# Kernel optimization log

Measured on AMD Instinct MI355X. Metric: run time of the kernel, lower is better.

The kernel has to match this reference:

```python
import jax, jax.numpy as jnp
import numpy as np

B, N, F = 2, 512, 64
LN_EPS = 1e-6

def _ln(x, scale, bias):
    mu = jnp.mean(x, axis=-1, keepdims=True)
    var = jnp.mean(jnp.square(x - mu), axis=-1, keepdims=True)
    return (x - mu) * jax.lax.rsqrt(var + LN_EPS) * scale + bias

def setup_inputs() -> dict:
    key = jax.random.key(0)
    k = jax.random.split(key, 16)
    w = lambda kk, s: jax.random.normal(kk, s, jnp.float32) * 0.02
    return {
        'qs': jax.random.normal(k[0], (B, N, F), jnp.float32),
        'ks': jax.random.normal(k[1], (B, N, F), jnp.float32),
        'vs': jax.random.normal(k[2], (B, N, F), jnp.float32),
        'qs_s': jax.random.normal(k[3], (B, N, 2), jnp.float32),
        'ks_s': jax.random.normal(k[4], (B, N, 2), jnp.float32),
        'qs_t': jax.random.uniform(k[5], (B, N, 1), dtype=jnp.float32),
        'ks_t': jax.random.uniform(k[6], (B, N, 1), dtype=jnp.float32),
        'valid_lens': jax.random.randint(k[7], (B,), 1, N + 1),
        'Wv': w(k[8], (F, 64)), 'bv': jnp.zeros((64,), jnp.float32),
        'Wa1': w(k[9], (2 * F + 5, 256)), 'ba1': jnp.zeros((256,), jnp.float32),
        'Wa2': w(k[10], (256, 256)), 'ba2': jnp.zeros((256,), jnp.float32),
        'Wa3': w(k[11], (256, 1)), 'ba3': jnp.zeros((1,), jnp.float32),
        'Wg1': w(k[12], (64, 256)), 'bg1': jnp.zeros((256,), jnp.float32),
        'Wg2': w(k[13], (256, 64)), 'bg2': jnp.zeros((64,), jnp.float32),
        'ln1_s': jnp.ones((64,), jnp.float32), 'ln1_b': jnp.zeros((64,), jnp.float32),
        'ln2_s': jnp.ones((64,), jnp.float32), 'ln2_b': jnp.zeros((64,), jnp.float32),
    }

def reference(qs, ks, vs, qs_s, ks_s, qs_t, ks_t, valid_lens,
              Wv, bv, Wa1, ba1, Wa2, ba2, Wa3, ba3,
              Wg1, bg1, Wg2, bg2, ln1_s, ln1_b, ln2_s, ln2_b):
    Bb, Q, Ff = qs.shape
    K = ks.shape[1]
    # pairwise broadcast-concat features: (B, Q, K, 2F+5)
    qb = jnp.broadcast_to(qs[:, :, None, :], (Bb, Q, K, Ff))
    kb = jnp.broadcast_to(ks[:, None, :, :], (Bb, Q, K, Ff))
    s_diff = qs_s[:, :, None, :] - ks_s[:, None, :, :]            # (B,Q,K,2)
    s_dist = jnp.linalg.norm(s_diff, axis=-1, keepdims=True)      # (B,Q,K,1)
    t_diff = qs_t[:, :, None, :] - ks_t[:, None, :, :]            # (B,Q,K,1)
    m = jnp.concatenate([qb, kb, s_diff, s_dist, jnp.square(s_dist), t_diff], axis=-1)
    # validity mask over the node axis (Q == K node-set attention)
    v_mask = (jnp.arange(K)[None, :] < valid_lens[:, None])[..., None]  # (B,K,1)
    mask = jnp.logical_and(v_mask, t_diff[..., 0] > 0)                   # (B,Q,K)
    # per-pair MLP attention score
    h = jax.nn.gelu(m @ Wa1 + ba1)
    h = jax.nn.gelu(h @ Wa2 + ba2)
    attn = (h @ Wa3 + ba3)[..., 0]                                       # (B,Q,K)
    attn = jnp.where(mask, attn, 0.0)
    vproj = vs @ Wv + bv                                                 # (B,K,64)
    ctx = _ln(jnp.einsum('bqk,bkd->bqd', attn, vproj), ln1_s, ln1_b)     # (B,Q,64)
    gate = jax.nn.gelu(ctx @ Wg1 + bg1) @ Wg2 + bg2                      # (B,Q,64)
    pooled = jnp.max(jnp.where(v_mask, gate * ctx, -jnp.inf), axis=1)    # (B,64)
    vnode = _ln(pooled, ln2_s, ln2_b)
    return ctx, vnode
```

## Files before the change

kernel.cpp:

```cpp
#include <hip/hip_runtime.h>
#include <math.h>

#define BB 2
#define NN 512
#define FF 64
#define HH 256
#define LN_EPS 1e-6f

typedef __attribute__((ext_vector_type(8))) short short8v;
typedef __attribute__((ext_vector_type(4))) float float4v;

#define LDAH 264

__device__ __forceinline__ float gelu_tanh(float x) {
    float x2 = x * x;
    float t  = __builtin_fmaf(0.10294340f, x2, 2.30211830f);
    float e  = exp2f(x * t);
    float r  = __builtin_amdgcn_rcpf(e + 1.0f);
    return __builtin_fmaf(-x, r, x);
}

__device__ __forceinline__ unsigned short f2bf(float f) {
    unsigned u = __float_as_uint(f);
    unsigned r = u + 0x7fffu + ((u >> 16) & 1u);
    return (unsigned short)(r >> 16);
}

__global__ __launch_bounds__(256) void prep_kernel(
    const float* __restrict__ qs, const float* __restrict__ ks,
    const float* __restrict__ vs,
    const float* __restrict__ Wa1, const float* __restrict__ ba1,
    const float* __restrict__ Wv,  const float* __restrict__ bv,
    const float* __restrict__ Wa2,
    const float* __restrict__ qs_t, const float* __restrict__ ks_t,
    const int*   __restrict__ valid_lens,
    float* __restrict__ Aq, float* __restrict__ Ak,
    float* __restrict__ vproj, unsigned short* __restrict__ Wa2T,
    int* __restrict__ klist, int* __restrict__ wl_count, int* __restrict__ wl,
    float* __restrict__ ctx_zero) {
    __shared__ int s_cnt[8];
    __shared__ int s_off[9];
    const int bid = blockIdx.x;
    const int t   = threadIdx.x;
    if (bid < 1024) {
        int idx = bid * 256 + t;
        int j  = idx & (HH - 1);
        int bn = idx >> 8;
        const float* qrow = qs + bn * FF;
        const float* krow = ks + bn * FF;
        float aq = ba1[j];
        float ak = 0.0f;
#pragma unroll 8
        for (int f = 0; f < FF; ++f) {
            aq += qrow[f] * Wa1[f * HH + j];
            ak += krow[f] * Wa1[(FF + f) * HH + j];
        }
        Aq[idx] = aq;
        Ak[idx] = ak;
    } else if (bid < 1280) {
        int idx = (bid - 1024) * 256 + t;
        int d  = idx & 63;
        int bn = idx >> 6;
        const float* vrow = vs + bn * FF;
        float a = bv[d];
#pragma unroll 8
        for (int f = 0; f < FF; ++f) a += vrow[f] * Wv[f * 64 + d];
        vproj[idx] = a;
        ctx_zero[idx] = 0.0f;
    } else if (bid < 1536) {
        int idx = (bid - 1280) * 256 + t;
        int n = idx >> 8;
        int i = idx & 255;
        Wa2T[idx] = f2bf(Wa2[i * HH + n]);
    } else {
        const int bq = bid - 1536;
        const int b  = bq >> 9;
        const int q  = bq & 511;
        if (q >= valid_lens[b]) return;
        const float qt = qs_t[bq];
        const int lane = t & 63;
        const int w    = t >> 6;
        bool validr[2];
        int  posr[2];
#pragma unroll
        for (int r = 0; r < 2; ++r) {
            int k = r * 256 + t;
            float kt = ks_t[b * NN + k];
            bool valid = (qt - kt) > 0.0f;
            unsigned long long bal = __ballot(valid);
            validr[r] = valid;
            posr[r] = (int)__popcll(bal & ((1ull << lane) - 1ull));
            if (lane == 0) s_cnt[r * 4 + w] = (int)__popcll(bal);
        }
        __syncthreads();
        if (t == 0) {
            int acc = 0;
#pragma unroll
            for (int i = 0; i < 8; ++i) { s_off[i] = acc; acc += s_cnt[i]; }
            s_off[8] = acc;
        }
        __syncthreads();
#pragma unroll
        for (int r = 0; r < 2; ++r)
            if (validr[r])
                klist[bq * 512 + s_off[r * 4 + w] + posr[r]] = r * 256 + t;
        const int nk = s_off[8];
        if (t == 0 && nk > 0) {
            int nch = (nk + 63) >> 6;
            int base = atomicAdd(wl_count, nch);
            for (int c = 0; c < nch; ++c) {
                int nv = nk - (c << 6);
                nv = nv > 64 ? 64 : nv;
                wl[base + c] = bq | (c << 10) | (nv << 13);
            }
        }
    }
}

__global__ __launch_bounds__(256, 3) void attn_ctx_kernel(
    const float* __restrict__ ks_s, const float* __restrict__ qs_s,
    const float* __restrict__ qs_t, const float* __restrict__ ks_t,
    const float* __restrict__ Wa1,
    const unsigned short* __restrict__ Wa2T,
    const float* __restrict__ ba2, const float* __restrict__ Wa3,
    const float* __restrict__ ba3,
    const float* __restrict__ Aq,  const float* __restrict__ Ak,
    const float* __restrict__ vproj,
    const int* __restrict__ klist, const int* __restrict__ wl_count,
    const int* __restrict__ wl,
    float* __restrict__ ctx_acc_g) {

    __shared__ unsigned short s_h1[64 * LDAH];
    __shared__ float4 s_feat4[64];
    __shared__ int    s_koe[64];
    __shared__ int    s_kvo[64];
    __shared__ float  s_part[4 * 64];
    __shared__ float  s_attn[64];

    const int i = blockIdx.x;
    if (i >= wl_count[0]) return;

    const int t    = threadIdx.x;
    const int lane = t & 63;
    const int w    = t >> 6;
    const int l15  = lane & 15;
    const int quad = lane >> 4;

    const int e  = wl[i];
    const int bq = e & 1023;
    const int c  = (e >> 10) & 7;
    const int nv = (e >> 13) & 127;
    const int b  = bq >> 9;

    const int n0 = w * 64;
    const unsigned short* bbase = Wa2T + (size_t)(n0 + l15) * HH + quad * 8;
    short8v Bcur[4];
#pragma unroll
    for (int nt = 0; nt < 4; ++nt)
        Bcur[nt] = *(const short8v*)(bbase + (size_t)nt * 16 * HH);

    const float qt   = qs_t[bq];
    const float qss0 = qs_s[bq * 2 + 0];
    const float qss1 = qs_s[bq * 2 + 1];
    if (t < 64) {
        int k = klist[bq * 512 + c * 64 + ((t < nv) ? t : 0)];
        int bk = b * NN + k;
        float d0 = qss0 - ks_s[bk * 2 + 0];
        float d1 = qss1 - ks_s[bk * 2 + 1];
        float dist = sqrtf(d0 * d0 + d1 * d1);
        float td = qt - ks_t[bk];
        s_feat4[t] = make_float4(d0, d1, dist, td);
        s_koe[t] = bk * HH;
        s_kvo[t] = bk * 64;
    }
    __syncthreads();

    {
        const int j = t;
        const float aq_j = Aq[bq * HH + j];
        const float wx0 = Wa1[128 * HH + j];
        const float wx1 = Wa1[129 * HH + j];
        const float wx2 = Wa1[130 * HH + j];
        const float wx3 = Wa1[131 * HH + j];
        const float wx4 = Wa1[132 * HH + j];
        const float* __restrict__ Akj = Ak + j;
#pragma unroll
        for (int g = 0; g < 8; ++g) {
            float akv[8];
#pragma unroll
            for (int u = 0; u < 8; ++u)
                akv[u] = Akj[s_koe[g * 8 + u]];
#pragma unroll
            for (int u = 0; u < 8; ++u) {
                int kl = g * 8 + u;
                float4 f = s_feat4[kl];
                float v = aq_j + akv[u] + wx0 * f.x + wx1 * f.y + wx2 * f.z
                        + wx3 * (f.z * f.z) + wx4 * f.w;
                s_h1[kl * LDAH + j] = f2bf(gelu_tanh(v));
            }
        }
    }
    __syncthreads();

    float4v acc[4][4];
#pragma unroll
    for (int mt = 0; mt < 4; ++mt)
#pragma unroll
        for (int nt = 0; nt < 4; ++nt) acc[mt][nt] = (float4v){0.f, 0.f, 0.f, 0.f};
    const unsigned short* abase = s_h1 + l15 * LDAH + quad * 8;
#pragma unroll
    for (int ksx = 0; ksx < 8; ++ksx) {
        short8v Bnxt[4];
        if (ksx < 7) {
            const int k1 = (ksx + 1) * 32;
#pragma unroll
            for (int nt = 0; nt < 4; ++nt)
                Bnxt[nt] = *(const short8v*)(bbase + (size_t)nt * 16 * HH + k1);
        }
        short8v Af[4];
        const int k0 = ksx * 32;
#pragma unroll
        for (int mt = 0; mt < 4; ++mt)
            Af[mt] = *(const short8v*)(abase + mt * 16 * LDAH + k0);
#pragma unroll
        for (int mt = 0; mt < 4; ++mt)
#pragma unroll
            for (int nt = 0; nt < 4; ++nt)
                acc[mt][nt] = __builtin_amdgcn_mfma_f32_16x16x32_bf16(
                    Af[mt], Bcur[nt], acc[mt][nt], 0, 0, 0);
        if (ksx < 7) {
#pragma unroll
            for (int nt = 0; nt < 4; ++nt) Bcur[nt] = Bnxt[nt];
        }
    }

    {
        float ba2r[4], wa3r[4];
#pragma unroll
        for (int nt = 0; nt < 4; ++nt) {
            int col = n0 + nt * 16 + l15;
            ba2r[nt] = ba2[col];
            wa3r[nt] = Wa3[col];
        }
        float prow[4][4];
#pragma unroll
        for (int mt = 0; mt < 4; ++mt)
#pragma unroll
            for (int r = 0; r < 4; ++r) prow[mt][r] = 0.0f;
#pragma unroll
        for (int mt = 0; mt < 4; ++mt)
#pragma unroll
            for (int nt = 0; nt < 4; ++nt)
#pragma unroll
                for (int r = 0; r < 4; ++r)
                    prow[mt][r] += gelu_tanh(acc[mt][nt][r] + ba2r[nt]) * wa3r[nt];
#pragma unroll
        for (int m = 1; m < 16; m <<= 1)
#pragma unroll
            for (int mt = 0; mt < 4; ++mt)
#pragma unroll
                for (int r = 0; r < 4; ++r)
                    prow[mt][r] += __shfl_xor(prow[mt][r], m);
        if (l15 == 0) {
#pragma unroll
            for (int mt = 0; mt < 4; ++mt)
#pragma unroll
                for (int r = 0; r < 4; ++r)
                    s_part[w * 64 + mt * 16 + quad * 4 + r] = prow[mt][r];
        }
    }
    __syncthreads();

    if (t < 64) {
        float a = 0.0f;
        if (t < nv)
            a = s_part[t] + s_part[64 + t] + s_part[128 + t] + s_part[192 + t] + ba3[0];
        s_attn[t] = a;
    }
    __syncthreads();

    {
        float cacc = 0.0f;
#pragma unroll
        for (int g = 0; g < 2; ++g) {
            float vv[8];
#pragma unroll
            for (int u = 0; u < 8; ++u)
                vv[u] = vproj[s_kvo[w * 16 + g * 8 + u] + lane];
#pragma unroll
            for (int u = 0; u < 8; ++u)
                cacc += s_attn[w * 16 + g * 8 + u] * vv[u];
        }
        s_part[w * 64 + lane] = cacc;
    }
    __syncthreads();
    if (t < 64) {
        float v = s_part[t] + s_part[64 + t] + s_part[128 + t] + s_part[192 + t];
        atomicAdd(&ctx_acc_g[bq * 64 + t], v);
    }
}

__global__ __launch_bounds__(256) void gate_kernel(
    float* __restrict__ ctx,
    const float* __restrict__ ln1_s, const float* __restrict__ ln1_b,
    const float* __restrict__ Wg1, const float* __restrict__ bg1,
    const float* __restrict__ Wg2, const float* __restrict__ bg2,
    const int* __restrict__ valid_lens,
    float* __restrict__ gctx) {
    __shared__ float s_ctx[64];
    __shared__ float s_hg[256];
    const int t  = threadIdx.x;
    const int bq = blockIdx.x;
    const int b  = bq >> 9;
    const int q  = bq & 511;
    if (t < 64) {
        float x = ctx[bq * 64 + t];
        float s = x;
#pragma unroll
        for (int m = 1; m < 64; m <<= 1) s += __shfl_xor(s, m);
        float mu = s * (1.0f / 64.0f);
        float dv = x - mu;
        float vv = dv * dv;
#pragma unroll
        for (int m = 1; m < 64; m <<= 1) vv += __shfl_xor(vv, m);
        float rs = rsqrtf(vv * (1.0f / 64.0f) + LN_EPS);
        float y = dv * rs * ln1_s[t] + ln1_b[t];
        ctx[bq * 64 + t] = y;
        s_ctx[t] = y;
    }
    __syncthreads();
    float a = bg1[t];
#pragma unroll 8
    for (int d = 0; d < 64; ++d) a += s_ctx[d] * Wg1[d * 256 + t];
    s_hg[t] = gelu_tanh(a);
    __syncthreads();
    if (t < 64) {
        float g = bg2[t];
#pragma unroll 8
        for (int jj = 0; jj < 256; ++jj) g += s_hg[jj] * Wg2[jj * 64 + t];
        float val = g * s_ctx[t];
        if (q >= valid_lens[b]) val = -INFINITY;
        gctx[bq * 64 + t] = val;
    }
}

__global__ __launch_bounds__(256) void pool_kernel(
    const float* __restrict__ gctx,
    const float* __restrict__ ln2_s, const float* __restrict__ ln2_b,
    float* __restrict__ vnode_out) {
    __shared__ float s_red[4 * 64];
    const int t = threadIdx.x;
    const int b = blockIdx.x;
    const int d = t & 63;
    const int g = t >> 6;
    float m = -INFINITY;
#pragma unroll 4
    for (int q = g; q < NN; q += 4)
        m = fmaxf(m, gctx[(b * NN + q) * 64 + d]);
    s_red[g * 64 + d] = m;
    __syncthreads();
    if (t < 64) {
        float x = fmaxf(fmaxf(s_red[t], s_red[64 + t]),
                        fmaxf(s_red[128 + t], s_red[192 + t]));
        float s = x;
#pragma unroll
        for (int mm = 1; mm < 64; mm <<= 1) s += __shfl_xor(s, mm);
        float mu = s * (1.0f / 64.0f);
        float dv = x - mu;
        float vv = dv * dv;
#pragma unroll
        for (int mm = 1; mm < 64; mm <<= 1) vv += __shfl_xor(vv, mm);
        float rs = rsqrtf(vv * (1.0f / 64.0f) + LN_EPS);
        vnode_out[b * 64 + t] = dv * rs * ln2_s[t] + ln2_b[t];
    }
}

extern "C" void kernel_launch(void* const* d_in, const int* in_sizes, int n_in,
                              void* d_out, int out_size, void* d_ws, size_t ws_size,
                              hipStream_t stream) {
    const float* qs   = (const float*)d_in[0];
    const float* ks   = (const float*)d_in[1];
    const float* vs   = (const float*)d_in[2];
    const float* qs_s = (const float*)d_in[3];
    const float* ks_s = (const float*)d_in[4];
    const float* qs_t = (const float*)d_in[5];
    const float* ks_t = (const float*)d_in[6];
    const int*   valid_lens = (const int*)d_in[7];
    const float* Wv   = (const float*)d_in[8];
    const float* bv   = (const float*)d_in[9];
    const float* Wa1  = (const float*)d_in[10];
    const float* ba1  = (const float*)d_in[11];
    const float* Wa2  = (const float*)d_in[12];
    const float* ba2  = (const float*)d_in[13];
    const float* Wa3  = (const float*)d_in[14];
    const float* ba3  = (const float*)d_in[15];
    const float* Wg1  = (const float*)d_in[16];
    const float* bg1  = (const float*)d_in[17];
    const float* Wg2  = (const float*)d_in[18];
    const float* bg2  = (const float*)d_in[19];
    const float* ln1_s = (const float*)d_in[20];
    const float* ln1_b = (const float*)d_in[21];
    const float* ln2_s = (const float*)d_in[22];
    const float* ln2_b = (const float*)d_in[23];

    float* out = (float*)d_out;
    float* ws  = (float*)d_ws;
    float* Aq    = ws;
    float* Ak    = Aq + BB * NN * HH;
    float* vproj = Ak + BB * NN * HH;
    float* gctx  = vproj + BB * NN * 64;
    unsigned short* Wa2T = (unsigned short*)(gctx + BB * NN * 64);
    int* klist = (int*)(Wa2T + HH * HH);
    int* wl_count = klist + BB * NN * 512;
    int* wl       = wl_count + 64;

    hipMemsetAsync(wl_count, 0, 64 * sizeof(int), stream);
    prep_kernel<<<2560, 256, 0, stream>>>(qs, ks, vs, Wa1, ba1, Wv, bv, Wa2,
                                          qs_t, ks_t, valid_lens,
                                          Aq, Ak, vproj, Wa2T, klist, wl_count, wl, out);
    attn_ctx_kernel<<<8192, 256, 0, stream>>>(ks_s, qs_s, qs_t, ks_t,
                                              Wa1, Wa2T, ba2, Wa3, ba3,
                                              Aq, Ak, vproj,
                                              klist, wl_count, wl, out);
    gate_kernel<<<BB * NN, 256, 0, stream>>>(out, ln1_s, ln1_b, Wg1, bg1, Wg2, bg2,
                                             valid_lens, gctx);
    pool_kernel<<<BB, 256, 0, stream>>>(gctx, ln2_s, ln2_b, out + BB * NN * 64);
}
```

Before: 227.8 us.

## Fuse max-pool into gate kernel via atomicMax, vectorize h1 build, use fast intrinsics

```diff
diff --git a/kernel.cpp b/kernel.cpp
--- a/kernel.cpp
+++ b/kernel.cpp
@@ -12,10 +12,21 @@
 
 #define LDAH 264
 
+#if __has_builtin(__builtin_amdgcn_exp2f)
+#define EXP2F(x) __builtin_amdgcn_exp2f(x)
+#else
+#define EXP2F(x) exp2f(x)
+#endif
+#if __has_builtin(__builtin_amdgcn_sqrtf)
+#define SQRTF(x) __builtin_amdgcn_sqrtf(x)
+#else
+#define SQRTF(x) sqrtf(x)
+#endif
+
 __device__ __forceinline__ float gelu_tanh(float x) {
     float x2 = x * x;
     float t  = __builtin_fmaf(0.10294340f, x2, 2.30211830f);
-    float e  = exp2f(x * t);
+    float e  = EXP2F(x * t);
     float r  = __builtin_amdgcn_rcpf(e + 1.0f);
     return __builtin_fmaf(-x, r, x);
 }
@@ -24,6 +35,14 @@
     unsigned u = __float_as_uint(f);
     unsigned r = u + 0x7fffu + ((u >> 16) & 1u);
     return (unsigned short)(r >> 16);
+}
+
+__device__ __forceinline__ unsigned enc_f(float f) {
+    unsigned b = __float_as_uint(f);
+    return (b & 0x80000000u) ? ~b : (b | 0x80000000u);
+}
+__device__ __forceinline__ float dec_f(unsigned u) {
+    return __uint_as_float((u & 0x80000000u) ? (u ^ 0x80000000u) : ~u);
 }
 
 __global__ __launch_bounds__(256) void prep_kernel(
@@ -167,7 +186,7 @@
         int bk = b * NN + k;
         float d0 = qss0 - ks_s[bk * 2 + 0];
         float d1 = qss1 - ks_s[bk * 2 + 1];
-        float dist = sqrtf(d0 * d0 + d1 * d1);
+        float dist = SQRTF(d0 * d0 + d1 * d1);
         float td = qt - ks_t[bk];
         s_feat4[t] = make_float4(d0, d1, dist, td);
         s_koe[t] = bk * HH;
@@ -176,27 +195,35 @@
     __syncthreads();
 
     {
-        const int j = t;
-        const float aq_j = Aq[bq * HH + j];
-        const float wx0 = Wa1[128 * HH + j];
-        const float wx1 = Wa1[129 * HH + j];
-        const float wx2 = Wa1[130 * HH + j];
-        const float wx3 = Wa1[131 * HH + j];
-        const float wx4 = Wa1[132 * HH + j];
-        const float* __restrict__ Akj = Ak + j;
-#pragma unroll
-        for (int g = 0; g < 8; ++g) {
-            float akv[8];
+        const int jp = (t & 127) * 2;
+        const int kh = (t >> 7) * 32;
+        const float2 aqv = *(const float2*)(Aq + bq * HH + jp);
+        const float2 w0v = *(const float2*)(Wa1 + 128 * HH + jp);
+        const float2 w1v = *(const float2*)(Wa1 + 129 * HH + jp);
+        const float2 w2v = *(const float2*)(Wa1 + 130 * HH + jp);
+        const float2 w3v = *(const float2*)(Wa1 + 131 * HH + jp);
+        const float2 w4v = *(const float2*)(Wa1 + 132 * HH + jp);
+        const float* __restrict__ Akj = Ak + jp;
+        unsigned* __restrict__ s_h1w = (unsigned*)s_h1;
+        const int colw = t & 127;
+#pragma unroll
+        for (int g = 0; g < 4; ++g) {
+            float2 akv[8];
 #pragma unroll
             for (int u = 0; u < 8; ++u)
-                akv[u] = Akj[s_koe[g * 8 + u]];
+                akv[u] = *(const float2*)(Akj + s_koe[kh + g * 8 + u]);
 #pragma unroll
             for (int u = 0; u < 8; ++u) {
-                int kl = g * 8 + u;
+                const int kl = kh + g * 8 + u;
                 float4 f = s_feat4[kl];
-                float v = aq_j + akv[u] + wx0 * f.x + wx1 * f.y + wx2 * f.z
-                        + wx3 * (f.z * f.z) + wx4 * f.w;
-                s_h1[kl * LDAH + j] = f2bf(gelu_tanh(v));
+                float fz2 = f.z * f.z;
+                float v0 = aqv.x + akv[u].x + w0v.x * f.x + w1v.x * f.y
+                         + w2v.x * f.z + w3v.x * fz2 + w4v.x * f.w;
+                float v1 = aqv.y + akv[u].y + w0v.y * f.x + w1v.y * f.y
+                         + w2v.y * f.z + w3v.y * fz2 + w4v.y * f.w;
+                unsigned lo = f2bf(gelu_tanh(v0));
+                unsigned hi = f2bf(gelu_tanh(v1));
+                s_h1w[kl * (LDAH / 2) + colw] = lo | (hi << 16);
             }
         }
     }
@@ -306,7 +333,7 @@
     const float* __restrict__ Wg1, const float* __restrict__ bg1,
     const float* __restrict__ Wg2, const float* __restrict__ bg2,
     const int* __restrict__ valid_lens,
-    float* __restrict__ gctx) {
+    unsigned* __restrict__ pooled) {
     __shared__ float s_ctx[64];
     __shared__ float s_hg[256];
     const int t  = threadIdx.x;
@@ -329,6 +356,7 @@
         s_ctx[t] = y;
     }
     __syncthreads();
+    if (q >= valid_lens[b]) return;
     float a = bg1[t];
 #pragma unroll 8
     for (int d = 0; d < 64; ++d) a += s_ctx[d] * Wg1[d * 256 + t];
@@ -338,41 +366,27 @@
         float g = bg2[t];
 #pragma unroll 8
         for (int jj = 0; jj < 256; ++jj) g += s_hg[jj] * Wg2[jj * 64 + t];
-        float val = g * s_ctx[t];
-        if (q >= valid_lens[b]) val = -INFINITY;
-        gctx[bq * 64 + t] = val;
-    }
-}
-
-__global__ __launch_bounds__(256) void pool_kernel(
-    const float* __restrict__ gctx,
+        atomicMax(&pooled[b * 64 + t], enc_f(g * s_ctx[t]));
+    }
+}
+
+__global__ __launch_bounds__(64) void ln2_kernel(
+    const unsigned* __restrict__ pooled,
     const float* __restrict__ ln2_s, const float* __restrict__ ln2_b,
     float* __restrict__ vnode_out) {
-    __shared__ float s_red[4 * 64];
     const int t = threadIdx.x;
     const int b = blockIdx.x;
-    const int d = t & 63;
-    const int g = t >> 6;
-    float m = -INFINITY;
-#pragma unroll 4
-    for (int q = g; q < NN; q += 4)
-        m = fmaxf(m, gctx[(b * NN + q) * 64 + d]);
-    s_red[g * 64 + d] = m;
-    __syncthreads();
-    if (t < 64) {
-        float x = fmaxf(fmaxf(s_red[t], s_red[64 + t]),
-                        fmaxf(s_red[128 + t], s_red[192 + t]));
-        float s = x;
-#pragma unroll
-        for (int mm = 1; mm < 64; mm <<= 1) s += __shfl_xor(s, mm);
-        float mu = s * (1.0f / 64.0f);
-        float dv = x - mu;
-        float vv = dv * dv;
-#pragma unroll
-        for (int mm = 1; mm < 64; mm <<= 1) vv += __shfl_xor(vv, mm);
-        float rs = rsqrtf(vv * (1.0f / 64.0f) + LN_EPS);
-        vnode_out[b * 64 + t] = dv * rs * ln2_s[t] + ln2_b[t];
-    }
+    float x = dec_f(pooled[b * 64 + t]);
+    float s = x;
+#pragma unroll
+    for (int mm = 1; mm < 64; mm <<= 1) s += __shfl_xor(s, mm);
+    float mu = s * (1.0f / 64.0f);
+    float dv = x - mu;
+    float vv = dv * dv;
+#pragma unroll
+    for (int mm = 1; mm < 64; mm <<= 1) vv += __shfl_xor(vv, mm);
+    float rs = rsqrtf(vv * (1.0f / 64.0f) + LN_EPS);
+    vnode_out[b * 64 + t] = dv * rs * ln2_s[t] + ln2_b[t];
 }
 
 extern "C" void kernel_launch(void* const* d_in, const int* in_sizes, int n_in,
@@ -408,13 +422,13 @@
     float* Aq    = ws;
     float* Ak    = Aq + BB * NN * HH;
     float* vproj = Ak + BB * NN * HH;
-    float* gctx  = vproj + BB * NN * 64;
-    unsigned short* Wa2T = (unsigned short*)(gctx + BB * NN * 64);
+    unsigned short* Wa2T = (unsigned short*)(vproj + BB * NN * 64);
     int* klist = (int*)(Wa2T + HH * HH);
     int* wl_count = klist + BB * NN * 512;
-    int* wl       = wl_count + 64;
-
-    hipMemsetAsync(wl_count, 0, 64 * sizeof(int), stream);
+    unsigned* pooled = (unsigned*)(wl_count + 64);
+    int* wl = (int*)(pooled + 128);
+
+    hipMemsetAsync(wl_count, 0, 192 * sizeof(int), stream);
     prep_kernel<<<2560, 256, 0, stream>>>(qs, ks, vs, Wa1, ba1, Wv, bv, Wa2,
                                           qs_t, ks_t, valid_lens,
                                           Aq, Ak, vproj, Wa2T, klist, wl_count, wl, out);
@@ -423,6 +437,6 @@
                                               Aq, Ak, vproj,
                                               klist, wl_count, wl, out);
     gate_kernel<<<BB * NN, 256, 0, stream>>>(out, ln1_s, ln1_b, Wg1, bg1, Wg2, bg2,
-                                             valid_lens, gctx);
-    pool_kernel<<<BB, 256, 0, stream>>>(gctx, ln2_s, ln2_b, out + BB * NN * 64);
-}
+                                             valid_lens, pooled);
+    ln2_kernel<<<BB, 64, 0, stream>>>(pooled, ln2_s, ln2_b, out + BB * NN * 64);
+}
```

New measurement: 204.6 us. -10.2%, faster.
